# Kernel optimization log

Hardware: AMD Instinct MI355X
Metric: run time of the kernel (lower is better)

The kernel has to match this reference:

```python
import jax, jax.numpy as jnp
import numpy as np

B, S, D, H, DK, DV = 4, 2048, 512, 8, 64, 64


def setup_inputs() -> dict:
    key0 = jax.random.key(0)
    ks = jax.random.split(key0, 11)
    w = 0.02
    return {
        "query": jax.random.normal(ks[0], (B, S, D), dtype=jnp.float32),
        "key": jax.random.normal(ks[1], (B, S, D), dtype=jnp.float32),
        "value": jax.random.normal(ks[2], (B, S, D), dtype=jnp.float32),
        "Wq": jax.random.normal(ks[3], (D, DK), dtype=jnp.float32) * w,
        "bq": jnp.zeros((DK,), dtype=jnp.float32),
        "Wk": jax.random.normal(ks[4], (D, DK), dtype=jnp.float32) * w,
        "bk": jnp.zeros((DK,), dtype=jnp.float32),
        "Wv": jax.random.normal(ks[5], (D, DV), dtype=jnp.float32) * w,
        "bv": jnp.zeros((DV,), dtype=jnp.float32),
        "Wo": jax.random.normal(ks[6], (H * DV, D), dtype=jnp.float32) * w,
        "bo": jnp.zeros((D,), dtype=jnp.float32),
    }


def reference(query, key, value, Wq, bq, Wk, bk, Wv, bv, Wo, bo):
    # NOTE: original module applies the SAME Dense layers to every head
    # (q_list = [self.query(query) for _ in range(heads)]), so all H heads
    # are mathematically identical -> compute one head and replicate.
    # NOTE: V is projected from `key`, not `value` (faithful to source bug).
    q = query @ Wq + bq          # [B, S, DK]
    k = key @ Wk + bk            # [B, S, DK]
    v = key @ Wv + bv            # [B, S, DV]
    scale = np.sqrt(DK).astype(np.float32)
    scores = jnp.einsum("bqd,bkd->bqk", q, k) / scale  # [B, S, S]
    # masked_mha=True and training=True -> causal mask, fill -1e19
    causal = jnp.triu(jnp.ones((S, S), dtype=scores.dtype), 1)
    scores = scores + causal * jnp.asarray(-1e19, scores.dtype)
    attn = jax.nn.softmax(scores, axis=-1)              # [B, S, S]
    o = jnp.einsum("bqk,bkv->bqv", attn, v)             # [B, S, DV]
    # concat of H identical heads along last axis == tile
    concat = jnp.tile(o, (1, 1, H))                     # [B, S, H*DV]
    return concat @ Wo + bo                             # [B, S, D]
```

## Files before the change

kernel.cpp:

```cpp
#include <hip/hip_runtime.h>
#include <hip/hip_bf16.h>


#define BB 4
#define SS 2048
#define BS (BB*SS)
#define MSHIFT 8.0f

typedef __bf16 v8bf __attribute__((ext_vector_type(8)));
typedef __bf16 v4bf __attribute__((ext_vector_type(4)));
typedef float  v4f  __attribute__((ext_vector_type(4)));

__device__ inline v8bf cvt8(float4 f0, float4 f1) {
    v8bf r;
    r[0] = (__bf16)f0.x; r[1] = (__bf16)f0.y; r[2] = (__bf16)f0.z; r[3] = (__bf16)f0.w;
    r[4] = (__bf16)f1.x; r[5] = (__bf16)f1.y; r[6] = (__bf16)f1.z; r[7] = (__bf16)f1.w;
    return r;
}

__global__ __launch_bounds__(512) void prep_kernel(
    const float* __restrict__ Wq, const float* __restrict__ bq,
    const float* __restrict__ Wk, const float* __restrict__ bk,
    const float* __restrict__ Wv, const float* __restrict__ bv,
    const float* __restrict__ Wo,
    __bf16* __restrict__ Wt, float* __restrict__ bs,
    __bf16* __restrict__ WoEt)
{
    const int t = threadIdx.x, y = blockIdx.y;
    const int idx = blockIdx.x * 512 + t;
    if (y < 3) {
        const float* W  = (y == 0) ? Wq : (y == 1) ? Wk : Wv;
        const float* bb = (y == 0) ? bq : (y == 1) ? bk : bv;
        const float s = (y == 0) ? (0.125f * 1.44269504088896340736f) : 1.0f;
        int c = idx & 63, k = idx >> 6;
        Wt[y * 32768 + c * 512 + k] = (__bf16)(W[k * 64 + c] * s);
        if (blockIdx.x == 0 && t < 64) bs[y * 64 + t] = bb[t] * s;
    } else {
        int d = idx & 511, k = idx >> 9;
        float sum = 0.f;
#pragma unroll
        for (int h = 0; h < 8; h++) sum += Wo[(size_t)(h * 64 + k) * 512 + d];
        WoEt[d * 64 + k] = (__bf16)sum;
    }
}

__global__ __launch_bounds__(256) void proj_kernel(
    const float* __restrict__ query, const float* __restrict__ key,
    const __bf16* __restrict__ Wt, const float* __restrict__ bs,
    __bf16* __restrict__ Qp, __bf16* __restrict__ Kp, __bf16* __restrict__ Vt)
{
    const int t = threadIdx.x;
    const int gw = (blockIdx.x * 256 + t) >> 6;
    const int lane = t & 63, lq = lane & 15, quad = lane >> 4;
    const int kind = gw >> 11;
    const int rr  = gw & 2047;
    const int rows = (rr >> 2) * 16;
    const int cb   = (rr & 3) * 16;
    const float* arow = ((kind == 0) ? query : key) + (size_t)(rows + lq) * 512;

    if (kind == 0) {
        const __bf16* W = Wt + (cb + lq) * 512;
        const float bb = bs[cb + lq];
        v4f acc = {bb, bb, bb, bb};
#pragma unroll 4
        for (int k0 = 0; k0 < 512; k0 += 32) {
            float4 f0 = *(const float4*)(arow + k0 + quad * 8);
            float4 f1 = *(const float4*)(arow + k0 + quad * 8 + 4);
            v8bf a = cvt8(f0, f1);
            v8bf b = *(const v8bf*)(W + k0 + quad * 8);
            acc = __builtin_amdgcn_mfma_f32_16x16x32_bf16(a, b, acc, 0, 0, 0);
        }
#pragma unroll
        for (int r = 0; r < 4; r++)
            Qp[(size_t)(rows + quad * 4 + r) * 64 + cb + lq] = (__bf16)acc[r];
    } else {
        const __bf16* Wk_ = Wt + 32768  + (cb + lq) * 512;
        const __bf16* Wv_ = Wt + 65536  + (cb + lq) * 512;
        const float bk_ = bs[64 + cb + lq], bv_ = bs[128 + cb + lq];
        v4f ak = {bk_, bk_, bk_, bk_}, av = {bv_, bv_, bv_, bv_};
#pragma unroll 4
        for (int k0 = 0; k0 < 512; k0 += 32) {
            float4 f0 = *(const float4*)(arow + k0 + quad * 8);
            float4 f1 = *(const float4*)(arow + k0 + quad * 8 + 4);
            v8bf a  = cvt8(f0, f1);
            v8bf b0 = *(const v8bf*)(Wk_ + k0 + quad * 8);
            v8bf b1 = *(const v8bf*)(Wv_ + k0 + quad * 8);
            ak = __builtin_amdgcn_mfma_f32_16x16x32_bf16(a, b0, ak, 0, 0, 0);
            av = __builtin_amdgcn_mfma_f32_16x16x32_bf16(a, b1, av, 0, 0, 0);
        }
#pragma unroll
        for (int r = 0; r < 4; r++)
            Kp[(size_t)(rows + quad * 4 + r) * 64 + cb + lq] = (__bf16)ak[r];
        v4bf o4; o4[0] = (__bf16)av[0]; o4[1] = (__bf16)av[1];
        o4[2] = (__bf16)av[2]; o4[3] = (__bf16)av[3];
        *(v4bf*)&Vt[(size_t)(cb + lq) * BS + rows + quad * 4] = o4;
    }
}

__global__ __launch_bounds__(256) void attn_kernel(
    const __bf16* __restrict__ Qp,
    const __bf16* __restrict__ Kp,
    const __bf16* __restrict__ Vt,
    __bf16* __restrict__ Opart,
    float* __restrict__ lpart,
    int nch)
{
    __shared__ __bf16 Ks[64][72];
    __shared__ __bf16 Vs[64][72];
    __shared__ __bf16 Ps[4][16][72];

    const int t    = threadIdx.x;
    const int lane = t & 63;
    const int w    = t >> 6;
    const int b    = blockIdx.x & 3;
    const int qt   = 31 - (blockIdx.x >> 2);
    const int c    = blockIdx.y;
    const int qbase = qt * 64;
    const int L    = qbase + 64;
    const int cs   = ((L + nch * 64 - 1) / (nch * 64)) * 64;
    const int klo  = c * cs;
    const int khi  = min(klo + cs, L);
    const size_t bbase = (size_t)b * SS;

    const int lq   = lane & 15;
    const int quad = lane >> 4;
    const int qrow_w = qbase + w * 16;
    const int wmax   = qrow_w + 15;

    const size_t qoff = (bbase + qrow_w + lq) * 64;
    v8bf qa0 = *(const v8bf*)(Qp + qoff + quad * 8);
    v8bf qa1 = *(const v8bf*)(Qp + qoff + 32 + quad * 8);

    v8bf ones;
#pragma unroll
    for (int i = 0; i < 8; i++) ones[i] = (__bf16)1.0f;

    v4f o[4] = {};
    v4f lacc = {};

    const int ky0 = t >> 3,         dd0 = (t & 7) * 8;
    const int ky1 = (t + 256) >> 3, dd1 = dd0;

    v8bf kpre0, kpre1, vpre0, vpre1;
    if (klo < khi) {
        kpre0 = *(const v8bf*)(Kp + (bbase + klo + ky0) * 64 + dd0);
        kpre1 = *(const v8bf*)(Kp + (bbase + klo + ky1) * 64 + dd1);
        vpre0 = *(const v8bf*)(Vt + (size_t)ky0 * BS + bbase + klo + dd0);
        vpre1 = *(const v8bf*)(Vt + (size_t)ky1 * BS + bbase + klo + dd1);
    }

    for (int kb = klo; kb < khi; kb += 64) {
        __syncthreads();
        *(v8bf*)&Ks[ky0][dd0] = kpre0;
        *(v8bf*)&Ks[ky1][dd1] = kpre1;
        *(v8bf*)&Vs[ky0][dd0] = vpre0;
        *(v8bf*)&Vs[ky1][dd1] = vpre1;
        if (kb + 64 < khi) {
            kpre0 = *(const v8bf*)(Kp + (bbase + kb + 64 + ky0) * 64 + dd0);
            kpre1 = *(const v8bf*)(Kp + (bbase + kb + 64 + ky1) * 64 + dd1);
            vpre0 = *(const v8bf*)(Vt + (size_t)ky0 * BS + bbase + kb + 64 + dd0);
            vpre1 = *(const v8bf*)(Vt + (size_t)ky1 * BS + bbase + kb + 64 + dd1);
        }
        __syncthreads();
        if (kb > wmax) continue;

        v4f s[4];
#pragma unroll
        for (int n = 0; n < 4; n++) {
            v8bf ka  = *(const v8bf*)&Ks[n * 16 + lq][quad * 8];
            v8bf kb2 = *(const v8bf*)&Ks[n * 16 + lq][32 + quad * 8];
            v4f z = {0.f, 0.f, 0.f, 0.f};
            z    = __builtin_amdgcn_mfma_f32_16x16x32_bf16(qa0, ka,  z, 0, 0, 0);
            s[n] = __builtin_amdgcn_mfma_f32_16x16x32_bf16(qa1, kb2, z, 0, 0, 0);
        }

        const int row0 = qrow_w + quad * 4;
        const int col0 = kb + lq;
#pragma unroll
        for (int n = 0; n < 4; n++)
#pragma unroll
            for (int r = 0; r < 4; r++) {
                float e = exp2f(s[n][r] - MSHIFT);
                e = (col0 + n * 16 > row0 + r) ? 0.f : e;
                Ps[w][quad * 4 + r][n * 16 + lq] = (__bf16)e;
            }
        v8bf pa0 = *(const v8bf*)&Ps[w][lq][quad * 8];
        v8bf pa1 = *(const v8bf*)&Ps[w][lq][32 + quad * 8];

        lacc = __builtin_amdgcn_mfma_f32_16x16x32_bf16(pa0, ones, lacc, 0, 0, 0);
        lacc = __builtin_amdgcn_mfma_f32_16x16x32_bf16(pa1, ones, lacc, 0, 0, 0);

#pragma unroll
        for (int vt = 0; vt < 4; vt++) {
            v8bf vb0 = *(const v8bf*)&Vs[vt * 16 + lq][quad * 8];
            v8bf vb1 = *(const v8bf*)&Vs[vt * 16 + lq][32 + quad * 8];
            o[vt] = __builtin_amdgcn_mfma_f32_16x16x32_bf16(pa0, vb0, o[vt], 0, 0, 0);
            o[vt] = __builtin_amdgcn_mfma_f32_16x16x32_bf16(pa1, vb1, o[vt], 0, 0, 0);
        }
    }

#pragma unroll
    for (int vt = 0; vt < 4; vt++)
#pragma unroll
        for (int r = 0; r < 4; r++) {
            int qrow = qrow_w + quad * 4 + r;
            Opart[((size_t)c * BS + bbase + qrow) * 64 + vt * 16 + lq] = (__bf16)o[vt][r];
        }
    if (lq < 4) {
        int qrow = qrow_w + quad * 4 + lq;
        lpart[(size_t)c * BS + bbase + qrow] = lacc[lq];
    }
}

__global__ __launch_bounds__(256) void outmerge_kernel(
    const __bf16* __restrict__ Opart, const float* __restrict__ lpart,
    const __bf16* __restrict__ WoEt, const float* __restrict__ bo,
    float* __restrict__ out, int nch)
{
    __shared__ __bf16 Os[16][72];
    const int t = threadIdx.x;
    const int rows0 = blockIdx.x * 16;
    {
        int row = t >> 4, d0 = (t & 15) * 4;
        float den = 0.f;
        for (int c = 0; c < nch; c++) den += lpart[(size_t)c * BS + rows0 + row];
        const float inv = 1.f / den;
        float a0 = 0.f, a1 = 0.f, a2 = 0.f, a3 = 0.f;
        for (int c = 0; c < nch; c++) {
            v4bf v = *(const v4bf*)&Opart[((size_t)c * BS + rows0 + row) * 64 + d0];
            a0 += (float)v[0]; a1 += (float)v[1]; a2 += (float)v[2]; a3 += (float)v[3];
        }
        Os[row][d0] = (__bf16)(a0 * inv); Os[row][d0 + 1] = (__bf16)(a1 * inv);
        Os[row][d0 + 2] = (__bf16)(a2 * inv); Os[row][d0 + 3] = (__bf16)(a3 * inv);
    }
    __syncthreads();

    const int lane = t & 63, lq = lane & 15, quad = lane >> 4;
    const int w = t >> 6;
    v8bf a0 = *(const v8bf*)&Os[lq][quad * 8];
    v8bf a1 = *(const v8bf*)&Os[lq][32 + quad * 8];
#pragma unroll
    for (int i = 0; i < 8; i++) {
        const int cb = (w * 8 + i) * 16;
        v8bf b0 = *(const v8bf*)(WoEt + (size_t)(cb + lq) * 64 + quad * 8);
        v8bf b1 = *(const v8bf*)(WoEt + (size_t)(cb + lq) * 64 + 32 + quad * 8);
        const float bb = bo[cb + lq];
        v4f acc = {bb, bb, bb, bb};
        acc = __builtin_amdgcn_mfma_f32_16x16x32_bf16(a0, b0, acc, 0, 0, 0);
        acc = __builtin_amdgcn_mfma_f32_16x16x32_bf16(a1, b1, acc, 0, 0, 0);
#pragma unroll
        for (int r = 0; r < 4; r++)
            out[(size_t)(rows0 + quad * 4 + r) * 512 + cb + lq] = acc[r];
    }
}

extern "C" void kernel_launch(void* const* d_in, const int* in_sizes, int n_in,
                              void* d_out, int out_size, void* d_ws, size_t ws_size,
                              hipStream_t stream) {
    const float* query = (const float*)d_in[0];
    const float* key   = (const float*)d_in[1];
    const float* Wq = (const float*)d_in[3];
    const float* bq = (const float*)d_in[4];
    const float* Wk = (const float*)d_in[5];
    const float* bk = (const float*)d_in[6];
    const float* Wv = (const float*)d_in[7];
    const float* bv = (const float*)d_in[8];
    const float* Wo = (const float*)d_in[9];
    const float* bo = (const float*)d_in[10];
    float* out = (float*)d_out;

    const int nch = (ws_size >= (size_t)12 * 1024 * 1024) ? 8 : 4;

    char* p = (char*)d_ws;
    __bf16* Qp    = (__bf16*)p; p += (size_t)BS * 64 * 2;
    __bf16* Kp    = (__bf16*)p; p += (size_t)BS * 64 * 2;
    __bf16* Vtg   = (__bf16*)p; p += (size_t)BS * 64 * 2;
    __bf16* Opart = (__bf16*)p; p += (size_t)nch * BS * 64 * 2;
    float* lpart = (float*)p;  p += (size_t)nch * BS * 4;
    __bf16* WoEt = (__bf16*)p; p += (size_t)64 * 512 * 2;
    __bf16* Wt   = (__bf16*)p; p += (size_t)3 * 64 * 512 * 2;
    float* bs    = (float*)p;  p += (size_t)3 * 64 * 4;

    prep_kernel<<<dim3(64, 4), 512, 0, stream>>>(Wq, bq, Wk, bk, Wv, bv, Wo, Wt, bs, WoEt);
    proj_kernel<<<1024, 256, 0, stream>>>(query, key, Wt, bs, Qp, Kp, Vtg);
    attn_kernel<<<dim3(128, nch), 256, 0, stream>>>(Qp, Kp, Vtg, Opart, lpart, nch);
    outmerge_kernel<<<512, 256, 0, stream>>>(Opart, lpart, WoEt, bo, out, nch);
}
```

Measured before the change: 149.9 us.

## Fuse all four stages into one persistent kernel with grid barriers

Replaces the four separate launches (weight prep, projection, chunked attention, merge plus output projection) with one persistent kernel. Its grid is sized to occupancy, and the stages are separated by a software grid barrier built on atomics in the workspace. This removes the launch overhead and tail gaps between kernels. In exchange it adds barrier spin costs and a memset per call. It relies on every block being co-resident, with no cooperative-launch guarantee, and the spin-loop timeout break could silently drop synchronisation.

```diff
diff --git a/kernel.cpp b/kernel.cpp
--- a/kernel.cpp
+++ b/kernel.cpp
@@ -6,6 +6,8 @@
 #define SS 2048
 #define BS (BB*SS)
 #define MSHIFT 8.0f
+#define NCH 8
+#define NVB 1024
 
 typedef __bf16 v8bf __attribute__((ext_vector_type(8)));
 typedef __bf16 v4bf __attribute__((ext_vector_type(4)));
@@ -18,239 +20,256 @@
     return r;
 }
 
-__global__ __launch_bounds__(512) void prep_kernel(
+__device__ __forceinline__ void grid_sync(unsigned* bar) {
+    __syncthreads();
+    if (threadIdx.x == 0) {
+        const unsigned nb = gridDim.x;
+        unsigned gen = __hip_atomic_load(&bar[1], __ATOMIC_RELAXED, __HIP_MEMORY_SCOPE_AGENT);
+        unsigned arr = __hip_atomic_fetch_add(&bar[0], 1u, __ATOMIC_ACQ_REL, __HIP_MEMORY_SCOPE_AGENT);
+        if (arr == nb - 1u) {
+            __hip_atomic_store(&bar[0], 0u, __ATOMIC_RELAXED, __HIP_MEMORY_SCOPE_AGENT);
+            __hip_atomic_store(&bar[1], gen + 1u, __ATOMIC_RELEASE, __HIP_MEMORY_SCOPE_AGENT);
+        } else {
+            unsigned spins = 0;
+            while (__hip_atomic_load(&bar[1], __ATOMIC_ACQUIRE, __HIP_MEMORY_SCOPE_AGENT) == gen) {
+                __builtin_amdgcn_s_sleep(1);
+                if (++spins > (1u << 22)) break;
+            }
+        }
+    }
+    __syncthreads();
+}
+
+__global__ __launch_bounds__(256) void fused_kernel(
+    const float* __restrict__ query, const float* __restrict__ key,
     const float* __restrict__ Wq, const float* __restrict__ bq,
     const float* __restrict__ Wk, const float* __restrict__ bk,
     const float* __restrict__ Wv, const float* __restrict__ bv,
-    const float* __restrict__ Wo,
-    __bf16* __restrict__ Wt, float* __restrict__ bs,
-    __bf16* __restrict__ WoEt)
-{
-    const int t = threadIdx.x, y = blockIdx.y;
-    const int idx = blockIdx.x * 512 + t;
-    if (y < 3) {
-        const float* W  = (y == 0) ? Wq : (y == 1) ? Wk : Wv;
-        const float* bb = (y == 0) ? bq : (y == 1) ? bk : bv;
-        const float s = (y == 0) ? (0.125f * 1.44269504088896340736f) : 1.0f;
-        int c = idx & 63, k = idx >> 6;
-        Wt[y * 32768 + c * 512 + k] = (__bf16)(W[k * 64 + c] * s);
-        if (blockIdx.x == 0 && t < 64) bs[y * 64 + t] = bb[t] * s;
-    } else {
-        int d = idx & 511, k = idx >> 9;
-        float sum = 0.f;
-#pragma unroll
-        for (int h = 0; h < 8; h++) sum += Wo[(size_t)(h * 64 + k) * 512 + d];
-        WoEt[d * 64 + k] = (__bf16)sum;
-    }
-}
-
-__global__ __launch_bounds__(256) void proj_kernel(
-    const float* __restrict__ query, const float* __restrict__ key,
-    const __bf16* __restrict__ Wt, const float* __restrict__ bs,
-    __bf16* __restrict__ Qp, __bf16* __restrict__ Kp, __bf16* __restrict__ Vt)
-{
-    const int t = threadIdx.x;
-    const int gw = (blockIdx.x * 256 + t) >> 6;
-    const int lane = t & 63, lq = lane & 15, quad = lane >> 4;
-    const int kind = gw >> 11;
-    const int rr  = gw & 2047;
-    const int rows = (rr >> 2) * 16;
-    const int cb   = (rr & 3) * 16;
-    const float* arow = ((kind == 0) ? query : key) + (size_t)(rows + lq) * 512;
-
-    if (kind == 0) {
-        const __bf16* W = Wt + (cb + lq) * 512;
-        const float bb = bs[cb + lq];
-        v4f acc = {bb, bb, bb, bb};
-#pragma unroll 4
-        for (int k0 = 0; k0 < 512; k0 += 32) {
-            float4 f0 = *(const float4*)(arow + k0 + quad * 8);
-            float4 f1 = *(const float4*)(arow + k0 + quad * 8 + 4);
-            v8bf a = cvt8(f0, f1);
-            v8bf b = *(const v8bf*)(W + k0 + quad * 8);
-            acc = __builtin_amdgcn_mfma_f32_16x16x32_bf16(a, b, acc, 0, 0, 0);
-        }
-#pragma unroll
-        for (int r = 0; r < 4; r++)
-            Qp[(size_t)(rows + quad * 4 + r) * 64 + cb + lq] = (__bf16)acc[r];
-    } else {
-        const __bf16* Wk_ = Wt + 32768  + (cb + lq) * 512;
-        const __bf16* Wv_ = Wt + 65536  + (cb + lq) * 512;
-        const float bk_ = bs[64 + cb + lq], bv_ = bs[128 + cb + lq];
-        v4f ak = {bk_, bk_, bk_, bk_}, av = {bv_, bv_, bv_, bv_};
-#pragma unroll 4
-        for (int k0 = 0; k0 < 512; k0 += 32) {
-            float4 f0 = *(const float4*)(arow + k0 + quad * 8);
-            float4 f1 = *(const float4*)(arow + k0 + quad * 8 + 4);
-            v8bf a  = cvt8(f0, f1);
-            v8bf b0 = *(const v8bf*)(Wk_ + k0 + quad * 8);
-            v8bf b1 = *(const v8bf*)(Wv_ + k0 + quad * 8);
-            ak = __builtin_amdgcn_mfma_f32_16x16x32_bf16(a, b0, ak, 0, 0, 0);
-            av = __builtin_amdgcn_mfma_f32_16x16x32_bf16(a, b1, av, 0, 0, 0);
-        }
-#pragma unroll
-        for (int r = 0; r < 4; r++)
-            Kp[(size_t)(rows + quad * 4 + r) * 64 + cb + lq] = (__bf16)ak[r];
-        v4bf o4; o4[0] = (__bf16)av[0]; o4[1] = (__bf16)av[1];
-        o4[2] = (__bf16)av[2]; o4[3] = (__bf16)av[3];
-        *(v4bf*)&Vt[(size_t)(cb + lq) * BS + rows + quad * 4] = o4;
-    }
-}
-
-__global__ __launch_bounds__(256) void attn_kernel(
-    const __bf16* __restrict__ Qp,
-    const __bf16* __restrict__ Kp,
-    const __bf16* __restrict__ Vt,
-    __bf16* __restrict__ Opart,
-    float* __restrict__ lpart,
-    int nch)
+    const float* __restrict__ Wo, const float* __restrict__ bo,
+    __bf16* __restrict__ Qp, __bf16* __restrict__ Kp, __bf16* __restrict__ Vt,
+    __bf16* __restrict__ Opart, float* __restrict__ lpart,
+    __bf16* __restrict__ WoEt, __bf16* __restrict__ Wt, float* __restrict__ bs,
+    float* __restrict__ out, unsigned* bar)
 {
     __shared__ __bf16 Ks[64][72];
     __shared__ __bf16 Vs[64][72];
     __shared__ __bf16 Ps[4][16][72];
 
     const int t    = threadIdx.x;
+    const int nb   = gridDim.x;
     const int lane = t & 63;
     const int w    = t >> 6;
-    const int b    = blockIdx.x & 3;
-    const int qt   = 31 - (blockIdx.x >> 2);
-    const int c    = blockIdx.y;
-    const int qbase = qt * 64;
-    const int L    = qbase + 64;
-    const int cs   = ((L + nch * 64 - 1) / (nch * 64)) * 64;
-    const int klo  = c * cs;
-    const int khi  = min(klo + cs, L);
-    const size_t bbase = (size_t)b * SS;
-
     const int lq   = lane & 15;
     const int quad = lane >> 4;
-    const int qrow_w = qbase + w * 16;
-    const int wmax   = qrow_w + 15;
-
-    const size_t qoff = (bbase + qrow_w + lq) * 64;
-    v8bf qa0 = *(const v8bf*)(Qp + qoff + quad * 8);
-    v8bf qa1 = *(const v8bf*)(Qp + qoff + 32 + quad * 8);
-
-    v8bf ones;
-#pragma unroll
-    for (int i = 0; i < 8; i++) ones[i] = (__bf16)1.0f;
-
-    v4f o[4] = {};
-    v4f lacc = {};
-
-    const int ky0 = t >> 3,         dd0 = (t & 7) * 8;
-    const int ky1 = (t + 256) >> 3, dd1 = dd0;
-
-    v8bf kpre0, kpre1, vpre0, vpre1;
-    if (klo < khi) {
-        kpre0 = *(const v8bf*)(Kp + (bbase + klo + ky0) * 64 + dd0);
-        kpre1 = *(const v8bf*)(Kp + (bbase + klo + ky1) * 64 + dd1);
-        vpre0 = *(const v8bf*)(Vt + (size_t)ky0 * BS + bbase + klo + dd0);
-        vpre1 = *(const v8bf*)(Vt + (size_t)ky1 * BS + bbase + klo + dd1);
-    }
-
-    for (int kb = klo; kb < khi; kb += 64) {
-        __syncthreads();
-        *(v8bf*)&Ks[ky0][dd0] = kpre0;
-        *(v8bf*)&Ks[ky1][dd1] = kpre1;
-        *(v8bf*)&Vs[ky0][dd0] = vpre0;
-        *(v8bf*)&Vs[ky1][dd1] = vpre1;
-        if (kb + 64 < khi) {
-            kpre0 = *(const v8bf*)(Kp + (bbase + kb + 64 + ky0) * 64 + dd0);
-            kpre1 = *(const v8bf*)(Kp + (bbase + kb + 64 + ky1) * 64 + dd1);
-            vpre0 = *(const v8bf*)(Vt + (size_t)ky0 * BS + bbase + kb + 64 + dd0);
-            vpre1 = *(const v8bf*)(Vt + (size_t)ky1 * BS + bbase + kb + 64 + dd1);
-        }
-        __syncthreads();
-        if (kb > wmax) continue;
-
-        v4f s[4];
-#pragma unroll
-        for (int n = 0; n < 4; n++) {
-            v8bf ka  = *(const v8bf*)&Ks[n * 16 + lq][quad * 8];
-            v8bf kb2 = *(const v8bf*)&Ks[n * 16 + lq][32 + quad * 8];
-            v4f z = {0.f, 0.f, 0.f, 0.f};
-            z    = __builtin_amdgcn_mfma_f32_16x16x32_bf16(qa0, ka,  z, 0, 0, 0);
-            s[n] = __builtin_amdgcn_mfma_f32_16x16x32_bf16(qa1, kb2, z, 0, 0, 0);
-        }
-
-        const int row0 = qrow_w + quad * 4;
-        const int col0 = kb + lq;
-#pragma unroll
-        for (int n = 0; n < 4; n++)
-#pragma unroll
-            for (int r = 0; r < 4; r++) {
-                float e = exp2f(s[n][r] - MSHIFT);
-                e = (col0 + n * 16 > row0 + r) ? 0.f : e;
-                Ps[w][quad * 4 + r][n * 16 + lq] = (__bf16)e;
-            }
-        v8bf pa0 = *(const v8bf*)&Ps[w][lq][quad * 8];
-        v8bf pa1 = *(const v8bf*)&Ps[w][lq][32 + quad * 8];
-
-        lacc = __builtin_amdgcn_mfma_f32_16x16x32_bf16(pa0, ones, lacc, 0, 0, 0);
-        lacc = __builtin_amdgcn_mfma_f32_16x16x32_bf16(pa1, ones, lacc, 0, 0, 0);
-
-#pragma unroll
-        for (int vt = 0; vt < 4; vt++) {
-            v8bf vb0 = *(const v8bf*)&Vs[vt * 16 + lq][quad * 8];
-            v8bf vb1 = *(const v8bf*)&Vs[vt * 16 + lq][32 + quad * 8];
-            o[vt] = __builtin_amdgcn_mfma_f32_16x16x32_bf16(pa0, vb0, o[vt], 0, 0, 0);
-            o[vt] = __builtin_amdgcn_mfma_f32_16x16x32_bf16(pa1, vb1, o[vt], 0, 0, 0);
-        }
-    }
-
-#pragma unroll
-    for (int vt = 0; vt < 4; vt++)
-#pragma unroll
-        for (int r = 0; r < 4; r++) {
-            int qrow = qrow_w + quad * 4 + r;
-            Opart[((size_t)c * BS + bbase + qrow) * 64 + vt * 16 + lq] = (__bf16)o[vt][r];
-        }
-    if (lq < 4) {
-        int qrow = qrow_w + quad * 4 + lq;
-        lpart[(size_t)c * BS + bbase + qrow] = lacc[lq];
-    }
-}
-
-__global__ __launch_bounds__(256) void outmerge_kernel(
-    const __bf16* __restrict__ Opart, const float* __restrict__ lpart,
-    const __bf16* __restrict__ WoEt, const float* __restrict__ bo,
-    float* __restrict__ out, int nch)
-{
-    __shared__ __bf16 Os[16][72];
-    const int t = threadIdx.x;
-    const int rows0 = blockIdx.x * 16;
+
+    for (int item = blockIdx.x * 256 + t; item < 131072; item += nb * 256) {
+        if (item < 98304) {
+            int y = item >> 15, idx = item & 32767;
+            const float* W  = (y == 0) ? Wq : (y == 1) ? Wk : Wv;
+            const float* bb = (y == 0) ? bq : (y == 1) ? bk : bv;
+            const float s = (y == 0) ? (0.125f * 1.44269504088896340736f) : 1.0f;
+            int c = idx & 63, k = idx >> 6;
+            Wt[y * 32768 + c * 512 + k] = (__bf16)(W[k * 64 + c] * s);
+            if (idx < 64) bs[y * 64 + idx] = bb[idx] * s;
+        } else {
+            int idx = item - 98304;
+            int d = idx & 511, k = idx >> 9;
+            float sum = 0.f;
+#pragma unroll
+            for (int h = 0; h < 8; h++) sum += Wo[(size_t)(h * 64 + k) * 512 + d];
+            WoEt[d * 64 + k] = (__bf16)sum;
+        }
+    }
+    grid_sync(bar);
+
+    for (int vb = blockIdx.x; vb < NVB; vb += nb) {
+        const int gw   = vb * 4 + w;
+        const int kind = gw >> 11;
+        const int rr   = gw & 2047;
+        const int rows = (rr >> 2) * 16;
+        const int cb   = (rr & 3) * 16;
+        const float* arow = ((kind == 0) ? query : key) + (size_t)(rows + lq) * 512;
+
+        if (kind == 0) {
+            const __bf16* W = Wt + (cb + lq) * 512;
+            const float bb = bs[cb + lq];
+            v4f acc = {bb, bb, bb, bb};
+#pragma unroll 4
+            for (int k0 = 0; k0 < 512; k0 += 32) {
+                float4 f0 = *(const float4*)(arow + k0 + quad * 8);
+                float4 f1 = *(const float4*)(arow + k0 + quad * 8 + 4);
+                v8bf a = cvt8(f0, f1);
+                v8bf b = *(const v8bf*)(W + k0 + quad * 8);
+                acc = __builtin_amdgcn_mfma_f32_16x16x32_bf16(a, b, acc, 0, 0, 0);
+            }
+#pragma unroll
+            for (int r = 0; r < 4; r++)
+                Qp[(size_t)(rows + quad * 4 + r) * 64 + cb + lq] = (__bf16)acc[r];
+        } else {
+            const __bf16* Wk_ = Wt + 32768 + (cb + lq) * 512;
+            const __bf16* Wv_ = Wt + 65536 + (cb + lq) * 512;
+            const float bk_ = bs[64 + cb + lq], bv_ = bs[128 + cb + lq];
+            v4f ak = {bk_, bk_, bk_, bk_}, av = {bv_, bv_, bv_, bv_};
+#pragma unroll 4
+            for (int k0 = 0; k0 < 512; k0 += 32) {
+                float4 f0 = *(const float4*)(arow + k0 + quad * 8);
+                float4 f1 = *(const float4*)(arow + k0 + quad * 8 + 4);
+                v8bf a  = cvt8(f0, f1);
+                v8bf b0 = *(const v8bf*)(Wk_ + k0 + quad * 8);
+                v8bf b1 = *(const v8bf*)(Wv_ + k0 + quad * 8);
+                ak = __builtin_amdgcn_mfma_f32_16x16x32_bf16(a, b0, ak, 0, 0, 0);
+                av = __builtin_amdgcn_mfma_f32_16x16x32_bf16(a, b1, av, 0, 0, 0);
+            }
+#pragma unroll
+            for (int r = 0; r < 4; r++)
+                Kp[(size_t)(rows + quad * 4 + r) * 64 + cb + lq] = (__bf16)ak[r];
+            v4bf o4; o4[0] = (__bf16)av[0]; o4[1] = (__bf16)av[1];
+            o4[2] = (__bf16)av[2]; o4[3] = (__bf16)av[3];
+            *(v4bf*)&Vt[(size_t)(cb + lq) * BS + rows + quad * 4] = o4;
+        }
+    }
+    grid_sync(bar);
+
     {
-        int row = t >> 4, d0 = (t & 15) * 4;
-        float den = 0.f;
-        for (int c = 0; c < nch; c++) den += lpart[(size_t)c * BS + rows0 + row];
-        const float inv = 1.f / den;
-        float a0 = 0.f, a1 = 0.f, a2 = 0.f, a3 = 0.f;
-        for (int c = 0; c < nch; c++) {
-            v4bf v = *(const v4bf*)&Opart[((size_t)c * BS + rows0 + row) * 64 + d0];
-            a0 += (float)v[0]; a1 += (float)v[1]; a2 += (float)v[2]; a3 += (float)v[3];
-        }
-        Os[row][d0] = (__bf16)(a0 * inv); Os[row][d0 + 1] = (__bf16)(a1 * inv);
-        Os[row][d0 + 2] = (__bf16)(a2 * inv); Os[row][d0 + 3] = (__bf16)(a3 * inv);
-    }
-    __syncthreads();
-
-    const int lane = t & 63, lq = lane & 15, quad = lane >> 4;
-    const int w = t >> 6;
-    v8bf a0 = *(const v8bf*)&Os[lq][quad * 8];
-    v8bf a1 = *(const v8bf*)&Os[lq][32 + quad * 8];
-#pragma unroll
-    for (int i = 0; i < 8; i++) {
-        const int cb = (w * 8 + i) * 16;
-        v8bf b0 = *(const v8bf*)(WoEt + (size_t)(cb + lq) * 64 + quad * 8);
-        v8bf b1 = *(const v8bf*)(WoEt + (size_t)(cb + lq) * 64 + 32 + quad * 8);
-        const float bb = bo[cb + lq];
-        v4f acc = {bb, bb, bb, bb};
-        acc = __builtin_amdgcn_mfma_f32_16x16x32_bf16(a0, b0, acc, 0, 0, 0);
-        acc = __builtin_amdgcn_mfma_f32_16x16x32_bf16(a1, b1, acc, 0, 0, 0);
-#pragma unroll
-        for (int r = 0; r < 4; r++)
-            out[(size_t)(rows0 + quad * 4 + r) * 512 + cb + lq] = acc[r];
+        v8bf ones;
+#pragma unroll
+        for (int i = 0; i < 8; i++) ones[i] = (__bf16)1.0f;
+
+        for (int vb = blockIdx.x; vb < NVB; vb += nb) {
+            const int x  = vb & 127;
+            const int ch = vb >> 7;
+            const int b  = x & 3;
+            const int qt = 31 - (x >> 2);
+            const int qbase = qt * 64;
+            const int L   = qbase + 64;
+            const int cs  = ((L + NCH * 64 - 1) / (NCH * 64)) * 64;
+            const int klo = ch * cs;
+            const int khi = min(klo + cs, L);
+            const size_t bbase = (size_t)b * SS;
+
+            const int qrow_w = qbase + w * 16;
+            const int wmax   = qrow_w + 15;
+
+            const size_t qoff = (bbase + qrow_w + lq) * 64;
+            v8bf qa0 = *(const v8bf*)(Qp + qoff + quad * 8);
+            v8bf qa1 = *(const v8bf*)(Qp + qoff + 32 + quad * 8);
+
+            v4f o[4] = {};
+            v4f lacc = {};
+
+            const int ky0 = t >> 3,         dd0 = (t & 7) * 8;
+            const int ky1 = (t + 256) >> 3, dd1 = dd0;
+
+            v8bf kpre0, kpre1, vpre0, vpre1;
+            if (klo < khi) {
+                kpre0 = *(const v8bf*)(Kp + (bbase + klo + ky0) * 64 + dd0);
+                kpre1 = *(const v8bf*)(Kp + (bbase + klo + ky1) * 64 + dd1);
+                vpre0 = *(const v8bf*)(Vt + (size_t)ky0 * BS + bbase + klo + dd0);
+                vpre1 = *(const v8bf*)(Vt + (size_t)ky1 * BS + bbase + klo + dd1);
+            }
+
+            for (int kb = klo; kb < khi; kb += 64) {
+                __syncthreads();
+                *(v8bf*)&Ks[ky0][dd0] = kpre0;
+                *(v8bf*)&Ks[ky1][dd1] = kpre1;
+                *(v8bf*)&Vs[ky0][dd0] = vpre0;
+                *(v8bf*)&Vs[ky1][dd1] = vpre1;
+                if (kb + 64 < khi) {
+                    kpre0 = *(const v8bf*)(Kp + (bbase + kb + 64 + ky0) * 64 + dd0);
+                    kpre1 = *(const v8bf*)(Kp + (bbase + kb + 64 + ky1) * 64 + dd1);
+                    vpre0 = *(const v8bf*)(Vt + (size_t)ky0 * BS + bbase + kb + 64 + dd0);
+                    vpre1 = *(const v8bf*)(Vt + (size_t)ky1 * BS + bbase + kb + 64 + dd1);
+                }
+                __syncthreads();
+                if (kb > wmax) continue;
+
+                v4f s[4];
+#pragma unroll
+                for (int n = 0; n < 4; n++) {
+                    v8bf ka  = *(const v8bf*)&Ks[n * 16 + lq][quad * 8];
+                    v8bf kb2 = *(const v8bf*)&Ks[n * 16 + lq][32 + quad * 8];
+                    v4f z = {0.f, 0.f, 0.f, 0.f};
+                    z    = __builtin_amdgcn_mfma_f32_16x16x32_bf16(qa0, ka,  z, 0, 0, 0);
+                    s[n] = __builtin_amdgcn_mfma_f32_16x16x32_bf16(qa1, kb2, z, 0, 0, 0);
+                }
+
+                const int row0 = qrow_w + quad * 4;
+                const int col0 = kb + lq;
+#pragma unroll
+                for (int n = 0; n < 4; n++)
+#pragma unroll
+                    for (int r = 0; r < 4; r++) {
+                        float e = exp2f(s[n][r] - MSHIFT);
+                        e = (col0 + n * 16 > row0 + r) ? 0.f : e;
+                        Ps[w][quad * 4 + r][n * 16 + lq] = (__bf16)e;
+                    }
+                v8bf pa0 = *(const v8bf*)&Ps[w][lq][quad * 8];
+                v8bf pa1 = *(const v8bf*)&Ps[w][lq][32 + quad * 8];
+
+                lacc = __builtin_amdgcn_mfma_f32_16x16x32_bf16(pa0, ones, lacc, 0, 0, 0);
+                lacc = __builtin_amdgcn_mfma_f32_16x16x32_bf16(pa1, ones, lacc, 0, 0, 0);
+
+#pragma unroll
+                for (int vt2 = 0; vt2 < 4; vt2++) {
+                    v8bf vb0 = *(const v8bf*)&Vs[vt2 * 16 + lq][quad * 8];
+                    v8bf vb1 = *(const v8bf*)&Vs[vt2 * 16 + lq][32 + quad * 8];
+                    o[vt2] = __builtin_amdgcn_mfma_f32_16x16x32_bf16(pa0, vb0, o[vt2], 0, 0, 0);
+                    o[vt2] = __builtin_amdgcn_mfma_f32_16x16x32_bf16(pa1, vb1, o[vt2], 0, 0, 0);
+                }
+            }
+
+#pragma unroll
+            for (int vt2 = 0; vt2 < 4; vt2++)
+#pragma unroll
+                for (int r = 0; r < 4; r++) {
+                    int qrow = qrow_w + quad * 4 + r;
+                    Opart[((size_t)ch * BS + bbase + qrow) * 64 + vt2 * 16 + lq] = (__bf16)o[vt2][r];
+                }
+            if (lq < 4) {
+                int qrow = qrow_w + quad * 4 + lq;
+                lpart[(size_t)ch * BS + bbase + qrow] = lacc[lq];
+            }
+        }
+    }
+    grid_sync(bar);
+
+    {
+        __bf16 (&Os)[64][72] = Ks;
+        for (int vb = blockIdx.x; vb < NVB; vb += nb) {
+            __syncthreads();
+            const int rows0 = (vb & 511) * 16;
+            const int half  = vb >> 9;
+            {
+                int row = t >> 4, d0 = (t & 15) * 4;
+                float den = 0.f;
+                for (int c2 = 0; c2 < NCH; c2++) den += lpart[(size_t)c2 * BS + rows0 + row];
+                const float inv = 1.f / den;
+                float a0 = 0.f, a1 = 0.f, a2 = 0.f, a3 = 0.f;
+                for (int c2 = 0; c2 < NCH; c2++) {
+                    v4bf v = *(const v4bf*)&Opart[((size_t)c2 * BS + rows0 + row) * 64 + d0];
+                    a0 += (float)v[0]; a1 += (float)v[1]; a2 += (float)v[2]; a3 += (float)v[3];
+                }
+                Os[row][d0] = (__bf16)(a0 * inv); Os[row][d0 + 1] = (__bf16)(a1 * inv);
+                Os[row][d0 + 2] = (__bf16)(a2 * inv); Os[row][d0 + 3] = (__bf16)(a3 * inv);
+            }
+            __syncthreads();
+
+            v8bf a0 = *(const v8bf*)&Os[lq][quad * 8];
+            v8bf a1 = *(const v8bf*)&Os[lq][32 + quad * 8];
+#pragma unroll
+            for (int i = 0; i < 4; i++) {
+                const int cb = (w * 8 + half * 4 + i) * 16;
+                v8bf b0 = *(const v8bf*)(WoEt + (size_t)(cb + lq) * 64 + quad * 8);
+                v8bf b1 = *(const v8bf*)(WoEt + (size_t)(cb + lq) * 64 + 32 + quad * 8);
+                const float bb = bo[cb + lq];
+                v4f acc = {bb, bb, bb, bb};
+                acc = __builtin_amdgcn_mfma_f32_16x16x32_bf16(a0, b0, acc, 0, 0, 0);
+                acc = __builtin_amdgcn_mfma_f32_16x16x32_bf16(a1, b1, acc, 0, 0, 0);
+#pragma unroll
+                for (int r = 0; r < 4; r++)
+                    out[(size_t)(rows0 + quad * 4 + r) * 512 + cb + lq] = acc[r];
+            }
+        }
     }
 }
 
@@ -269,20 +288,31 @@
     const float* bo = (const float*)d_in[10];
     float* out = (float*)d_out;
 
-    const int nch = (ws_size >= (size_t)12 * 1024 * 1024) ? 8 : 4;
-
     char* p = (char*)d_ws;
     __bf16* Qp    = (__bf16*)p; p += (size_t)BS * 64 * 2;
     __bf16* Kp    = (__bf16*)p; p += (size_t)BS * 64 * 2;
     __bf16* Vtg   = (__bf16*)p; p += (size_t)BS * 64 * 2;
-    __bf16* Opart = (__bf16*)p; p += (size_t)nch * BS * 64 * 2;
-    float* lpart = (float*)p;  p += (size_t)nch * BS * 4;
+    __bf16* Opart = (__bf16*)p; p += (size_t)NCH * BS * 64 * 2;
+    float* lpart = (float*)p;  p += (size_t)NCH * BS * 4;
     __bf16* WoEt = (__bf16*)p; p += (size_t)64 * 512 * 2;
     __bf16* Wt   = (__bf16*)p; p += (size_t)3 * 64 * 512 * 2;
-    float* bs    = (float*)p;  p += (size_t)3 * 64 * 4;
-
-    prep_kernel<<<dim3(64, 4), 512, 0, stream>>>(Wq, bq, Wk, bk, Wv, bv, Wo, Wt, bs, WoEt);
-    proj_kernel<<<1024, 256, 0, stream>>>(query, key, Wt, bs, Qp, Kp, Vtg);
-    attn_kernel<<<dim3(128, nch), 256, 0, stream>>>(Qp, Kp, Vtg, Opart, lpart, nch);
-    outmerge_kernel<<<512, 256, 0, stream>>>(Opart, lpart, WoEt, bo, out, nch);
+    float* bs    = (float*)p;  p += 768;
+    uintptr_t pa = ((uintptr_t)p + 255) & ~(uintptr_t)255;
+    unsigned* bar = (unsigned*)pa;
+
+    static int nb_s = 0;
+    if (nb_s == 0) {
+        int perCU = 0;
+        if (hipOccupancyMaxActiveBlocksPerMultiprocessor(
+                &perCU, reinterpret_cast<const void*>(fused_kernel), 256, 0) != hipSuccess
+            || perCU < 1)
+            perCU = 1;
+        nb_s = perCU * 256;
+        if (nb_s > NVB) nb_s = NVB;
+    }
+
+    hipMemsetAsync(bar, 0, 64, stream);
+    fused_kernel<<<nb_s, 256, 0, stream>>>(
+        query, key, Wq, bq, Wk, bk, Wv, bv, Wo, bo,
+        Qp, Kp, Vtg, Opart, lpart, WoEt, Wt, bs, out, bar);
 }
```

New measurement: 258.3 us. 72.3% more time.

## Fuse weight prep into projection and merge+output projection into attention

Applied to the files above, without the earlier changes.

Folds the weight transpose/cast into the projection kernel, where each block stages its weight slice in shared memory. The split-K merge and Wo projection move into the attention kernel: an atomic arrival counter per query tile lets the last-arriving chunk block do the reduction and the output GEMM. This drops two kernel launches and the global round trip through the prepped weights, at the cost of a memset, redundant per-block weight conversion, serialized tail work in the last block, and a fixed 8-chunk split with no fallback for a smaller workspace.

```diff
diff --git a/kernel.cpp b/kernel.cpp
--- a/kernel.cpp
+++ b/kernel.cpp
@@ -6,6 +6,7 @@
 #define SS 2048
 #define BS (BB*SS)
 #define MSHIFT 8.0f
+#define NCH 8
 
 typedef __bf16 v8bf __attribute__((ext_vector_type(8)));
 typedef __bf16 v4bf __attribute__((ext_vector_type(4)));
@@ -18,73 +19,95 @@
     return r;
 }
 
-__global__ __launch_bounds__(512) void prep_kernel(
+__global__ __launch_bounds__(256) void projprep_kernel(
+    const float* __restrict__ query, const float* __restrict__ key,
     const float* __restrict__ Wq, const float* __restrict__ bq,
     const float* __restrict__ Wk, const float* __restrict__ bk,
     const float* __restrict__ Wv, const float* __restrict__ bv,
     const float* __restrict__ Wo,
-    __bf16* __restrict__ Wt, float* __restrict__ bs,
+    __bf16* __restrict__ Qp, __bf16* __restrict__ Kp, __bf16* __restrict__ Vt,
     __bf16* __restrict__ WoEt)
 {
-    const int t = threadIdx.x, y = blockIdx.y;
-    const int idx = blockIdx.x * 512 + t;
-    if (y < 3) {
-        const float* W  = (y == 0) ? Wq : (y == 1) ? Wk : Wv;
-        const float* bb = (y == 0) ? bq : (y == 1) ? bk : bv;
-        const float s = (y == 0) ? (0.125f * 1.44269504088896340736f) : 1.0f;
-        int c = idx & 63, k = idx >> 6;
-        Wt[y * 32768 + c * 512 + k] = (__bf16)(W[k * 64 + c] * s);
-        if (blockIdx.x == 0 && t < 64) bs[y * 64 + t] = bb[t] * s;
-    } else {
-        int d = idx & 511, k = idx >> 9;
-        float sum = 0.f;
-#pragma unroll
-        for (int h = 0; h < 8; h++) sum += Wo[(size_t)(h * 64 + k) * 512 + d];
-        WoEt[d * 64 + k] = (__bf16)sum;
-    }
-}
-
-__global__ __launch_bounds__(256) void proj_kernel(
-    const float* __restrict__ query, const float* __restrict__ key,
-    const __bf16* __restrict__ Wt, const float* __restrict__ bs,
-    __bf16* __restrict__ Qp, __bf16* __restrict__ Kp, __bf16* __restrict__ Vt)
-{
-    const int t = threadIdx.x;
-    const int gw = (blockIdx.x * 256 + t) >> 6;
-    const int lane = t & 63, lq = lane & 15, quad = lane >> 4;
-    const int kind = gw >> 11;
-    const int rr  = gw & 2047;
-    const int rows = (rr >> 2) * 16;
-    const int cb   = (rr & 3) * 16;
+    __shared__ __bf16 Ws[2][16][520];
+    const int t  = threadIdx.x;
+    const int vb = blockIdx.x;
+
+    if (vb >= 1024) {
+        const int k = vb - 1024;
+        for (int d = t; d < 512; d += 256) {
+            float sum = 0.f;
+#pragma unroll
+            for (int h = 0; h < 8; h++) sum += Wo[(size_t)(h * 64 + k) * 512 + d];
+            WoEt[d * 64 + k] = (__bf16)sum;
+        }
+        return;
+    }
+
+    const int lane = t & 63, w = t >> 6, lq = lane & 15, quad = lane >> 4;
+    const int kind = vb >> 9;
+    const int v2   = vb & 511;
+    const int cb   = (v2 & 3) * 16;
+    const int rows = (v2 >> 2) * 64 + w * 16;
+    const float qscale = 0.125f * 1.44269504088896340736f;
+
+    {
+        const int c4 = (t & 3) * 4;
+        const int kk = t >> 2;
+        if (kind == 0) {
+#pragma unroll
+            for (int pass = 0; pass < 8; pass++) {
+                int k = kk + pass * 64;
+                float4 f = *(const float4*)(Wq + (size_t)k * 64 + cb + c4);
+                Ws[0][c4 + 0][k] = (__bf16)(f.x * qscale);
+                Ws[0][c4 + 1][k] = (__bf16)(f.y * qscale);
+                Ws[0][c4 + 2][k] = (__bf16)(f.z * qscale);
+                Ws[0][c4 + 3][k] = (__bf16)(f.w * qscale);
+            }
+        } else {
+#pragma unroll
+            for (int pass = 0; pass < 8; pass++) {
+                int k = kk + pass * 64;
+                float4 fk = *(const float4*)(Wk + (size_t)k * 64 + cb + c4);
+                float4 fv = *(const float4*)(Wv + (size_t)k * 64 + cb + c4);
+                Ws[0][c4 + 0][k] = (__bf16)fk.x;
+                Ws[0][c4 + 1][k] = (__bf16)fk.y;
+                Ws[0][c4 + 2][k] = (__bf16)fk.z;
+                Ws[0][c4 + 3][k] = (__bf16)fk.w;
+                Ws[1][c4 + 0][k] = (__bf16)fv.x;
+                Ws[1][c4 + 1][k] = (__bf16)fv.y;
+                Ws[1][c4 + 2][k] = (__bf16)fv.z;
+                Ws[1][c4 + 3][k] = (__bf16)fv.w;
+            }
+        }
+    }
+    __syncthreads();
+
     const float* arow = ((kind == 0) ? query : key) + (size_t)(rows + lq) * 512;
 
     if (kind == 0) {
-        const __bf16* W = Wt + (cb + lq) * 512;
-        const float bb = bs[cb + lq];
+        const float bb = bq[cb + lq] * qscale;
         v4f acc = {bb, bb, bb, bb};
 #pragma unroll 4
         for (int k0 = 0; k0 < 512; k0 += 32) {
             float4 f0 = *(const float4*)(arow + k0 + quad * 8);
             float4 f1 = *(const float4*)(arow + k0 + quad * 8 + 4);
             v8bf a = cvt8(f0, f1);
-            v8bf b = *(const v8bf*)(W + k0 + quad * 8);
+            v8bf b = *(const v8bf*)&Ws[0][lq][k0 + quad * 8];
             acc = __builtin_amdgcn_mfma_f32_16x16x32_bf16(a, b, acc, 0, 0, 0);
         }
 #pragma unroll
         for (int r = 0; r < 4; r++)
             Qp[(size_t)(rows + quad * 4 + r) * 64 + cb + lq] = (__bf16)acc[r];
     } else {
-        const __bf16* Wk_ = Wt + 32768  + (cb + lq) * 512;
-        const __bf16* Wv_ = Wt + 65536  + (cb + lq) * 512;
-        const float bk_ = bs[64 + cb + lq], bv_ = bs[128 + cb + lq];
+        const float bk_ = bk[cb + lq], bv_ = bv[cb + lq];
         v4f ak = {bk_, bk_, bk_, bk_}, av = {bv_, bv_, bv_, bv_};
 #pragma unroll 4
         for (int k0 = 0; k0 < 512; k0 += 32) {
             float4 f0 = *(const float4*)(arow + k0 + quad * 8);
             float4 f1 = *(const float4*)(arow + k0 + quad * 8 + 4);
             v8bf a  = cvt8(f0, f1);
-            v8bf b0 = *(const v8bf*)(Wk_ + k0 + quad * 8);
-            v8bf b1 = *(const v8bf*)(Wv_ + k0 + quad * 8);
+            v8bf b0 = *(const v8bf*)&Ws[0][lq][k0 + quad * 8];
+            v8bf b1 = *(const v8bf*)&Ws[1][lq][k0 + quad * 8];
             ak = __builtin_amdgcn_mfma_f32_16x16x32_bf16(a, b0, ak, 0, 0, 0);
             av = __builtin_amdgcn_mfma_f32_16x16x32_bf16(a, b1, av, 0, 0, 0);
         }
@@ -103,11 +126,15 @@
     const __bf16* __restrict__ Vt,
     __bf16* __restrict__ Opart,
     float* __restrict__ lpart,
-    int nch)
+    const __bf16* __restrict__ WoEt,
+    const float* __restrict__ bo,
+    float* __restrict__ out,
+    unsigned* __restrict__ cnt)
 {
     __shared__ __bf16 Ks[64][72];
     __shared__ __bf16 Vs[64][72];
     __shared__ __bf16 Ps[4][16][72];
+    __shared__ unsigned arr_s;
 
     const int t    = threadIdx.x;
     const int lane = t & 63;
@@ -117,7 +144,7 @@
     const int c    = blockIdx.y;
     const int qbase = qt * 64;
     const int L    = qbase + 64;
-    const int cs   = ((L + nch * 64 - 1) / (nch * 64)) * 64;
+    const int cs   = ((L + NCH * 64 - 1) / (NCH * 64)) * 64;
     const int klo  = c * cs;
     const int khi  = min(klo + cs, L);
     const size_t bbase = (size_t)b * SS;
@@ -191,66 +218,74 @@
         lacc = __builtin_amdgcn_mfma_f32_16x16x32_bf16(pa1, ones, lacc, 0, 0, 0);
 
 #pragma unroll
-        for (int vt = 0; vt < 4; vt++) {
-            v8bf vb0 = *(const v8bf*)&Vs[vt * 16 + lq][quad * 8];
-            v8bf vb1 = *(const v8bf*)&Vs[vt * 16 + lq][32 + quad * 8];
-            o[vt] = __builtin_amdgcn_mfma_f32_16x16x32_bf16(pa0, vb0, o[vt], 0, 0, 0);
-            o[vt] = __builtin_amdgcn_mfma_f32_16x16x32_bf16(pa1, vb1, o[vt], 0, 0, 0);
-        }
-    }
-
-#pragma unroll
-    for (int vt = 0; vt < 4; vt++)
+        for (int vt2 = 0; vt2 < 4; vt2++) {
+            v8bf vb0 = *(const v8bf*)&Vs[vt2 * 16 + lq][quad * 8];
+            v8bf vb1 = *(const v8bf*)&Vs[vt2 * 16 + lq][32 + quad * 8];
+            o[vt2] = __builtin_amdgcn_mfma_f32_16x16x32_bf16(pa0, vb0, o[vt2], 0, 0, 0);
+            o[vt2] = __builtin_amdgcn_mfma_f32_16x16x32_bf16(pa1, vb1, o[vt2], 0, 0, 0);
+        }
+    }
+
+#pragma unroll
+    for (int vt2 = 0; vt2 < 4; vt2++)
 #pragma unroll
         for (int r = 0; r < 4; r++) {
             int qrow = qrow_w + quad * 4 + r;
-            Opart[((size_t)c * BS + bbase + qrow) * 64 + vt * 16 + lq] = (__bf16)o[vt][r];
+            Opart[((size_t)c * BS + bbase + qrow) * 64 + vt2 * 16 + lq] = (__bf16)o[vt2][r];
         }
     if (lq < 4) {
         int qrow = qrow_w + quad * 4 + lq;
         lpart[(size_t)c * BS + bbase + qrow] = lacc[lq];
     }
-}
-
-__global__ __launch_bounds__(256) void outmerge_kernel(
-    const __bf16* __restrict__ Opart, const float* __restrict__ lpart,
-    const __bf16* __restrict__ WoEt, const float* __restrict__ bo,
-    float* __restrict__ out, int nch)
-{
-    __shared__ __bf16 Os[16][72];
-    const int t = threadIdx.x;
-    const int rows0 = blockIdx.x * 16;
+
+    __syncthreads();
+    if (t == 0)
+        arr_s = __hip_atomic_fetch_add(&cnt[b * 32 + qt], 1u,
+                                       __ATOMIC_ACQ_REL, __HIP_MEMORY_SCOPE_AGENT);
+    __syncthreads();
+    if (arr_s != NCH - 1u) return;
+
+    __bf16 (&Os)[64][72] = Ks;
     {
-        int row = t >> 4, d0 = (t & 15) * 4;
+        const int row = t >> 2;
+        const int d0  = (t & 3) * 16;
+        const size_t grow = bbase + qbase + row;
         float den = 0.f;
-        for (int c = 0; c < nch; c++) den += lpart[(size_t)c * BS + rows0 + row];
+#pragma unroll
+        for (int c2 = 0; c2 < NCH; c2++) den += lpart[(size_t)c2 * BS + grow];
         const float inv = 1.f / den;
-        float a0 = 0.f, a1 = 0.f, a2 = 0.f, a3 = 0.f;
-        for (int c = 0; c < nch; c++) {
-            v4bf v = *(const v4bf*)&Opart[((size_t)c * BS + rows0 + row) * 64 + d0];
-            a0 += (float)v[0]; a1 += (float)v[1]; a2 += (float)v[2]; a3 += (float)v[3];
-        }
-        Os[row][d0] = (__bf16)(a0 * inv); Os[row][d0 + 1] = (__bf16)(a1 * inv);
-        Os[row][d0 + 2] = (__bf16)(a2 * inv); Os[row][d0 + 3] = (__bf16)(a3 * inv);
+        float m[16] = {0.f, 0.f, 0.f, 0.f, 0.f, 0.f, 0.f, 0.f,
+                       0.f, 0.f, 0.f, 0.f, 0.f, 0.f, 0.f, 0.f};
+#pragma unroll
+        for (int c2 = 0; c2 < NCH; c2++) {
+            const __bf16* src = Opart + ((size_t)c2 * BS + grow) * 64 + d0;
+            v8bf u0 = *(const v8bf*)src;
+            v8bf u1 = *(const v8bf*)(src + 8);
+#pragma unroll
+            for (int j = 0; j < 8; j++) { m[j] += (float)u0[j]; m[8 + j] += (float)u1[j]; }
+        }
+#pragma unroll
+        for (int j = 0; j < 16; j++) Os[row][d0 + j] = (__bf16)(m[j] * inv);
     }
     __syncthreads();
 
-    const int lane = t & 63, lq = lane & 15, quad = lane >> 4;
-    const int w = t >> 6;
-    v8bf a0 = *(const v8bf*)&Os[lq][quad * 8];
-    v8bf a1 = *(const v8bf*)&Os[lq][32 + quad * 8];
-#pragma unroll
-    for (int i = 0; i < 8; i++) {
-        const int cb = (w * 8 + i) * 16;
-        v8bf b0 = *(const v8bf*)(WoEt + (size_t)(cb + lq) * 64 + quad * 8);
-        v8bf b1 = *(const v8bf*)(WoEt + (size_t)(cb + lq) * 64 + 32 + quad * 8);
-        const float bb = bo[cb + lq];
-        v4f acc = {bb, bb, bb, bb};
-        acc = __builtin_amdgcn_mfma_f32_16x16x32_bf16(a0, b0, acc, 0, 0, 0);
-        acc = __builtin_amdgcn_mfma_f32_16x16x32_bf16(a1, b1, acc, 0, 0, 0);
-#pragma unroll
-        for (int r = 0; r < 4; r++)
-            out[(size_t)(rows0 + quad * 4 + r) * 512 + cb + lq] = acc[r];
+    {
+        v8bf a0 = *(const v8bf*)&Os[w * 16 + lq][quad * 8];
+        v8bf a1 = *(const v8bf*)&Os[w * 16 + lq][32 + quad * 8];
+        const int orow = qbase + w * 16;
+#pragma unroll 4
+        for (int i = 0; i < 32; i++) {
+            const int cb2 = i * 16;
+            v8bf b0 = *(const v8bf*)(WoEt + (size_t)(cb2 + lq) * 64 + quad * 8);
+            v8bf b1 = *(const v8bf*)(WoEt + (size_t)(cb2 + lq) * 64 + 32 + quad * 8);
+            const float bb2 = bo[cb2 + lq];
+            v4f acc = {bb2, bb2, bb2, bb2};
+            acc = __builtin_amdgcn_mfma_f32_16x16x32_bf16(a0, b0, acc, 0, 0, 0);
+            acc = __builtin_amdgcn_mfma_f32_16x16x32_bf16(a1, b1, acc, 0, 0, 0);
+#pragma unroll
+            for (int r = 0; r < 4; r++)
+                out[(size_t)(bbase + orow + quad * 4 + r) * 512 + cb2 + lq] = acc[r];
+        }
     }
 }
 
@@ -269,20 +304,19 @@
     const float* bo = (const float*)d_in[10];
     float* out = (float*)d_out;
 
-    const int nch = (ws_size >= (size_t)12 * 1024 * 1024) ? 8 : 4;
-
     char* p = (char*)d_ws;
     __bf16* Qp    = (__bf16*)p; p += (size_t)BS * 64 * 2;
     __bf16* Kp    = (__bf16*)p; p += (size_t)BS * 64 * 2;
     __bf16* Vtg   = (__bf16*)p; p += (size_t)BS * 64 * 2;
-    __bf16* Opart = (__bf16*)p; p += (size_t)nch * BS * 64 * 2;
-    float* lpart = (float*)p;  p += (size_t)nch * BS * 4;
+    __bf16* Opart = (__bf16*)p; p += (size_t)NCH * BS * 64 * 2;
+    float* lpart = (float*)p;  p += (size_t)NCH * BS * 4;
     __bf16* WoEt = (__bf16*)p; p += (size_t)64 * 512 * 2;
-    __bf16* Wt   = (__bf16*)p; p += (size_t)3 * 64 * 512 * 2;
-    float* bs    = (float*)p;  p += (size_t)3 * 64 * 4;
-
-    prep_kernel<<<dim3(64, 4), 512, 0, stream>>>(Wq, bq, Wk, bk, Wv, bv, Wo, Wt, bs, WoEt);
-    proj_kernel<<<1024, 256, 0, stream>>>(query, key, Wt, bs, Qp, Kp, Vtg);
-    attn_kernel<<<dim3(128, nch), 256, 0, stream>>>(Qp, Kp, Vtg, Opart, lpart, nch);
-    outmerge_kernel<<<512, 256, 0, stream>>>(Opart, lpart, WoEt, bo, out, nch);
+    uintptr_t pa = ((uintptr_t)p + 255) & ~(uintptr_t)255;
+    unsigned* cnt = (unsigned*)pa;
+
+    (void)hipMemsetAsync(cnt, 0, 512, stream);
+    projprep_kernel<<<1088, 256, 0, stream>>>(
+        query, key, Wq, bq, Wk, bk, Wv, bv, Wo, Qp, Kp, Vtg, WoEt);
+    attn_kernel<<<dim3(128, NCH), 256, 0, stream>>>(
+        Qp, Kp, Vtg, Opart, lpart, WoEt, bo, out, cnt);
 }
```

New measurement: 177.6 us. 18.5% more time.
